# Optimization experiments

Hardware: AMD Instinct MI355X
Metric: run time of the kernel (lower is better)

## Reference

```python
import jax, jax.numpy as jnp
import numpy as np

# Static graph layout: B equal-size graphs so per-graph k is static under jit.
B = 64          # number of graphs
N_PER = 1024    # nodes per graph
RATIO = 0.5
K = max(1, int(RATIO * N_PER))  # 512 nodes kept per graph
MULTIPLIER = 1.0
N = B * N_PER   # 65536 total nodes
E = 2_097_152   # total edges
F_IN = 256
F_E = 16


def setup_inputs() -> dict:
    key = jax.random.key(0)
    k1, k2, k3, k4 = jax.random.split(key, 4)
    x = jax.random.normal(k1, (N, F_IN), dtype=jnp.float32)
    edge_index = jax.random.randint(k2, (2, E), 0, N, dtype=jnp.int32)
    edge_attr = jax.random.normal(k3, (E, F_E), dtype=jnp.float32)
    batch = jnp.repeat(jnp.arange(B, dtype=jnp.int32), N_PER)  # sorted, equal sizes
    # Linear(in_channels, 1) params (PyTorch default init style)
    W = jax.random.uniform(k4, (1, F_IN), dtype=jnp.float32,
                           minval=-1.0, maxval=1.0) / jnp.sqrt(F_IN)
    b = jnp.zeros((1,), dtype=jnp.float32)
    return {"x": x, "edge_index": edge_index, "edge_attr": edge_attr,
            "batch": batch, "W": W, "b": b}


def reference(x, edge_index, edge_attr, batch, W, b):
    # score = multiplier * tanh(proj(x))  -> [N]
    score = MULTIPLIER * jnp.tanh(x @ W.T + b)[:, 0]

    # Per-graph top-k (graphs are contiguous, equal size -> reshape + top_k)
    _, idx = jax.lax.top_k(score.reshape(B, N_PER), K)        # [B, K], desc order
    offsets = (jnp.arange(B, dtype=idx.dtype) * N_PER)[:, None]
    perm = (idx + offsets).reshape(-1)                          # [B*K] global node ids
    batch_out = jnp.repeat(jnp.arange(B, dtype=batch.dtype), K)

    # Gate kept node features by their score
    x_out = x[perm] * score[perm][:, None]                      # [B*K, F_IN]

    # filter_adj: keep edges whose both endpoints survive, remap node ids
    mask = jnp.zeros((N,), dtype=bool).at[perm].set(True)
    row, col = edge_index[0], edge_index[1]
    edge_mask = mask[row] & mask[col]                           # [E]
    node_map = jnp.zeros((N,), dtype=jnp.int32).at[perm].set(
        jnp.arange(B * K, dtype=jnp.int32))
    # jit-friendly: fixed-size outputs; invalid edges marked -1 / zeroed
    ei_new = jnp.where(edge_mask[None, :], node_map[edge_index], -1)
    ea_new = jnp.where(edge_mask[:, None], edge_attr, 0.0)

    return (x_out, ei_new, ea_new, batch_out, perm, score, edge_mask)
```

## Files before the change

### kernel.cpp

```cpp
#include <hip/hip_runtime.h>
#include <math.h>

#define BGRAPH 64
#define N_PER  1024
#define KSEL   512
#define NTOT   65536
#define EDG    2097152
#define FIN    256
#define FE     16

#define OFF_XOUT   0
#define OFF_EI     8388608
#define OFF_EA     12582912
#define OFF_BATCH  46137344
#define OFF_PERM   46170112
#define OFF_SCORE  46202880
#define OFF_EMASK  46268416

__global__ __launch_bounds__(256) void score_kernel(
    const float* __restrict__ x, const float* __restrict__ W,
    const float* __restrict__ bptr, float* __restrict__ score_out) {
  int wave = threadIdx.x >> 6;
  int lane = threadIdx.x & 63;
  int node = blockIdx.x * 4 + wave;
  const float4* xr = reinterpret_cast<const float4*>(x + (size_t)node * FIN);
  const float4* wr = reinterpret_cast<const float4*>(W);
  float4 xv = xr[lane];
  float4 wv = wr[lane];
  double p = (double)xv.x * (double)wv.x + (double)xv.y * (double)wv.y +
             (double)xv.z * (double)wv.z + (double)xv.w * (double)wv.w;
#pragma unroll
  for (int off = 32; off >= 1; off >>= 1) p += __shfl_xor(p, off, 64);
  if (lane == 0) {
    double s = tanh(p + (double)bptr[0]);
    score_out[node] = (float)s;
  }
}

__global__ __launch_bounds__(1024) void topk_kernel(
    const float* __restrict__ score, float* __restrict__ perm_out,
    float* __restrict__ batch_out, int* __restrict__ node_map) {
  __shared__ float sk[N_PER];
  __shared__ int   si[N_PER];
  int b = blockIdx.x;
  int t = threadIdx.x;
  int base = b * N_PER;
  sk[t] = score[base + t];
  si[t] = t;
  node_map[base + t] = -1;
  __syncthreads();
  for (int k = 2; k <= N_PER; k <<= 1) {
    for (int j = k >> 1; j > 0; j >>= 1) {
      int ixj = t ^ j;
      if (ixj > t) {
        float a = sk[t], c = sk[ixj];
        int ia = si[t], ic = si[ixj];
        bool prec = (a > c) || (a == c && ia < ic);
        bool dirUp = ((t & k) == 0);
        bool doswap = dirUp ? !prec : prec;
        if (doswap) { sk[t] = c; sk[ixj] = a; si[t] = ic; si[ixj] = ia; }
      }
      __syncthreads();
    }
  }
  if (t < KSEL) {
    int g   = base + si[t];
    int gid = b * KSEL + t;
    perm_out[gid]  = (float)g;
    batch_out[gid] = (float)b;
    node_map[g]    = gid;
  }
}

__global__ __launch_bounds__(256) void gather_kernel(
    const float* __restrict__ x, const float* __restrict__ perm_f,
    const float* __restrict__ score, float* __restrict__ xout) {
  int wave = threadIdx.x >> 6;
  int lane = threadIdx.x & 63;
  int r = blockIdx.x * 4 + wave;
  int g = (int)perm_f[r];
  float s = score[g];
  float4 v = reinterpret_cast<const float4*>(x + (size_t)g * FIN)[lane];
  float4 o;
  o.x = v.x * s; o.y = v.y * s; o.z = v.z * s; o.w = v.w * s;
  reinterpret_cast<float4*>(xout + (size_t)r * FIN)[lane] = o;
}

__global__ __launch_bounds__(256) void edgeA_kernel(
    const int* __restrict__ ei, const int* __restrict__ node_map,
    float* __restrict__ ei_out, float* __restrict__ emask_out) {
  int e = blockIdx.x * 256 + threadIdx.x;
  int r = ei[e];
  int c = ei[EDG + e];
  int nr = node_map[r];
  int nc = node_map[c];
  bool m = (nr >= 0) && (nc >= 0);
  ei_out[e]       = m ? (float)nr : -1.0f;
  ei_out[EDG + e] = m ? (float)nc : -1.0f;
  emask_out[e]    = m ? 1.0f : 0.0f;
}

__global__ __launch_bounds__(256) void edgeB_kernel(
    const float* __restrict__ ea, const float* __restrict__ emask,
    float* __restrict__ ea_out) {
  int t = blockIdx.x * 256 + threadIdx.x;
  float m = emask[t >> 2];
  float4 v = make_float4(0.f, 0.f, 0.f, 0.f);
  if (m != 0.0f) v = reinterpret_cast<const float4*>(ea)[t];
  reinterpret_cast<float4*>(ea_out)[t] = v;
}

extern "C" void kernel_launch(void* const* d_in, const int* in_sizes, int n_in,
                              void* d_out, int out_size, void* d_ws, size_t ws_size,
                              hipStream_t stream) {
  const float* x  = (const float*)d_in[0];
  const int*   ei = (const int*)d_in[1];
  const float* ea = (const float*)d_in[2];
  const float* W  = (const float*)d_in[4];
  const float* bb = (const float*)d_in[5];

  float* out       = (float*)d_out;
  float* xout      = out + OFF_XOUT;
  float* ei_out    = out + OFF_EI;
  float* ea_out    = out + OFF_EA;
  float* batch_out = out + OFF_BATCH;
  float* perm_out  = out + OFF_PERM;
  float* score_out = out + OFF_SCORE;
  float* emask_out = out + OFF_EMASK;

  int* node_map = (int*)d_ws;

  score_kernel <<<NTOT / 4, 256, 0, stream>>>(x, W, bb, score_out);
  topk_kernel  <<<BGRAPH, 1024, 0, stream>>>(score_out, perm_out, batch_out, node_map);
  gather_kernel<<<(BGRAPH * KSEL) / 4, 256, 0, stream>>>(x, perm_out, score_out, xout);
  edgeA_kernel <<<EDG / 256, 256, 0, stream>>>(ei, node_map, ei_out, emask_out);
  edgeB_kernel <<<(EDG * 4) / 256, 256, 0, stream>>>(ea, emask_out, ea_out);
}
```

Measured before the change: 127.1 us.

## Fuse edge kernels and use wave shuffles in bitonic top-k sort

Merges the edge index/mask kernel and the edge-attribute masking kernel into one launch that shares the mask through LDS, avoiding a global re-read of the mask and one launch. The bitonic sort in top-k keeps key/index in registers and uses cross-lane shuffles for strides below the wave size, reducing shared-memory traffic and barriers. The fused edge kernel has only a quarter of threads doing index work per block, which may reduce memory-level parallelism for the gathers.

```diff
diff --git a/kernel.cpp b/kernel.cpp
--- a/kernel.cpp
+++ b/kernel.cpp
@@ -45,26 +45,30 @@
   int b = blockIdx.x;
   int t = threadIdx.x;
   int base = b * N_PER;
-  sk[t] = score[base + t];
-  si[t] = t;
+  float key = score[base + t];
+  int   idx = t;
   node_map[base + t] = -1;
-  __syncthreads();
   for (int k = 2; k <= N_PER; k <<= 1) {
     for (int j = k >> 1; j > 0; j >>= 1) {
-      int ixj = t ^ j;
-      if (ixj > t) {
-        float a = sk[t], c = sk[ixj];
-        int ia = si[t], ic = si[ixj];
-        bool prec = (a > c) || (a == c && ia < ic);
-        bool dirUp = ((t & k) == 0);
-        bool doswap = dirUp ? !prec : prec;
-        if (doswap) { sk[t] = c; sk[ixj] = a; si[t] = ic; si[ixj] = ia; }
+      bool lower = (t & j) == 0;
+      bool dirUp = (t & k) == 0;
+      float okey; int oidx;
+      if (j >= 64) {
+        sk[t] = key; si[t] = idx;
+        __syncthreads();
+        okey = sk[t ^ j]; oidx = si[t ^ j];
+        __syncthreads();
+      } else {
+        okey = __shfl_xor(key, j, 64);
+        oidx = __shfl_xor(idx, j, 64);
       }
-      __syncthreads();
+      bool own_prec = (key > okey) || (key == okey && idx < oidx);
+      bool want_prec = (lower == dirUp);
+      if (own_prec != want_prec) { key = okey; idx = oidx; }
     }
   }
   if (t < KSEL) {
-    int g   = base + si[t];
+    int g   = base + idx;
     int gid = b * KSEL + t;
     perm_out[gid]  = (float)g;
     batch_out[gid] = (float)b;
@@ -86,28 +90,32 @@
   reinterpret_cast<float4*>(xout + (size_t)r * FIN)[lane] = o;
 }
 
-__global__ __launch_bounds__(256) void edgeA_kernel(
+__global__ __launch_bounds__(256) void edge_kernel(
     const int* __restrict__ ei, const int* __restrict__ node_map,
-    float* __restrict__ ei_out, float* __restrict__ emask_out) {
-  int e = blockIdx.x * 256 + threadIdx.x;
-  int r = ei[e];
-  int c = ei[EDG + e];
-  int nr = node_map[r];
-  int nc = node_map[c];
-  bool m = (nr >= 0) && (nc >= 0);
-  ei_out[e]       = m ? (float)nr : -1.0f;
-  ei_out[EDG + e] = m ? (float)nc : -1.0f;
-  emask_out[e]    = m ? 1.0f : 0.0f;
-}
-
-__global__ __launch_bounds__(256) void edgeB_kernel(
-    const float* __restrict__ ea, const float* __restrict__ emask,
-    float* __restrict__ ea_out) {
-  int t = blockIdx.x * 256 + threadIdx.x;
-  float m = emask[t >> 2];
+    const float* __restrict__ ea, float* __restrict__ ei_out,
+    float* __restrict__ emask_out, float* __restrict__ ea_out) {
+  __shared__ float smask[64];
+  int base = blockIdx.x * 64;
+  int tid = threadIdx.x;
+  if (tid < 64) {
+    int e = base + tid;
+    int r = ei[e];
+    int c = ei[EDG + e];
+    int nr = node_map[r];
+    int nc = node_map[c];
+    bool m = (nr >= 0) && (nc >= 0);
+    ei_out[e]       = m ? (float)nr : -1.0f;
+    ei_out[EDG + e] = m ? (float)nc : -1.0f;
+    float mf = m ? 1.0f : 0.0f;
+    emask_out[e] = mf;
+    smask[tid]   = mf;
+  }
+  __syncthreads();
+  int q = base * 4 + tid;
+  float m = smask[tid >> 2];
   float4 v = make_float4(0.f, 0.f, 0.f, 0.f);
-  if (m != 0.0f) v = reinterpret_cast<const float4*>(ea)[t];
-  reinterpret_cast<float4*>(ea_out)[t] = v;
+  if (m != 0.0f) v = reinterpret_cast<const float4*>(ea)[q];
+  reinterpret_cast<float4*>(ea_out)[q] = v;
 }
 
 extern "C" void kernel_launch(void* const* d_in, const int* in_sizes, int n_in,
@@ -133,6 +141,5 @@
   score_kernel <<<NTOT / 4, 256, 0, stream>>>(x, W, bb, score_out);
   topk_kernel  <<<BGRAPH, 1024, 0, stream>>>(score_out, perm_out, batch_out, node_map);
   gather_kernel<<<(BGRAPH * KSEL) / 4, 256, 0, stream>>>(x, perm_out, score_out, xout);
-  edgeA_kernel <<<EDG / 256, 256, 0, stream>>>(ei, node_map, ei_out, emask_out);
-  edgeB_kernel <<<(EDG * 4) / 256, 256, 0, stream>>>(ea, emask_out, ea_out);
+  edge_kernel  <<<EDG / 64, 256, 0, stream>>>(ei, node_map, ea, ei_out, emask_out, ea_out);
 }
```

New measurement: 117.8 us. 1.08x faster.
